# Optimization experiments

Hardware: AMD Instinct MI355X
Metric: run time of the kernel (lower is better)

Reference implementation:

```python
import jax, jax.numpy as jnp
import numpy as np

EPS = 1e-6
TEMPERATURE = 0.1
NEG_INF = -1.0e9

B, S, H = 8, 1024, 1024
M = 16384  # memory_size


def setup_inputs() -> dict:
    key = jax.random.key(0)
    ks = jax.random.split(key, 10)
    sc = 1.0 / np.sqrt(H)
    return {
        "hidden_states": jax.random.normal(ks[0], (B, S, H), jnp.float32),
        "Wk": jax.random.normal(ks[1], (H, H), jnp.float32) * sc,
        "bk": jax.random.normal(ks[2], (H,), jnp.float32) * 0.01,
        "Wv": jax.random.normal(ks[3], (H, H), jnp.float32) * sc,
        "bv": jax.random.normal(ks[4], (H,), jnp.float32) * 0.01,
        "Wo": jax.random.normal(ks[5], (H, H), jnp.float32) * sc,
        "bo": jax.random.normal(ks[6], (H,), jnp.float32) * 0.01,
        "memory_keys": jax.random.normal(ks[7], (M, H), jnp.float32),
        "memory_values": jax.random.normal(ks[8], (M, H), jnp.float32),
        "memory_usage": jax.random.randint(ks[9], (M,), 0, 3, jnp.int32),
    }


def _normalize(x):
    # matches torch: x * rsqrt(sum(x^2) + 1e-6)
    return x * jax.lax.rsqrt(jnp.sum(jnp.square(x), axis=-1, keepdims=True) + EPS)


def reference(hidden_states, Wk, bk, Wv, bv, Wo, bo,
              memory_keys, memory_values, memory_usage):
    # key projection + L2-ish normalization of queries
    q = hidden_states @ Wk.T + bk              # [B,S,H]
    qn = _normalize(q)
    mkn = _normalize(memory_keys)              # [M,H]
    # cosine-similarity attention over memory slots
    scores = jnp.einsum('bsh,mh->bsm', qn, mkn) / TEMPERATURE  # [B,S,M]
    mask = (memory_usage > 0).astype(scores.dtype)             # [M]
    scores = scores * mask + NEG_INF * (1.0 - mask)
    w = jax.nn.softmax(scores, axis=-1)                        # [B,S,M]
    retrieved = jnp.einsum('bsm,mh->bsh', w, memory_values)    # [B,S,H]
    return retrieved @ Wo.T + bo
```

## Files before the change

### kernel.cpp

```cpp
#include <hip/hip_runtime.h>
#include <hip/hip_bf16.h>
#include <stdint.h>
#include <stddef.h>

typedef __bf16 bf16_t;
typedef __attribute__((ext_vector_type(8))) __bf16 bf16x8;
typedef __attribute__((ext_vector_type(4))) __bf16 bf16x4;
typedef __attribute__((ext_vector_type(4))) float f32x4;

#define HDIM 1024
#define MSLOTS 16384
#define NROWS 8192

__device__ __forceinline__ void load16_lds(const void* g, void* l) {
  __builtin_amdgcn_global_load_lds((const __attribute__((address_space(1))) void*)g,
                                   (__attribute__((address_space(3))) void*)l, 16, 0, 0);
}

__global__ void init_compact(int* __restrict__ cmask) {
  int i = blockIdx.x * blockDim.x + threadIdx.x;
  if (i < MSLOTS) cmask[i] = 0;
}

__global__ void compact_scan(const int* __restrict__ usage, int* __restrict__ posmap,
                             int* __restrict__ cmask, int* __restrict__ smalls) {
  __shared__ int wtot[16], wbase[16];
  const int t = threadIdx.x;
  const int lane = t & 63, wid = t >> 6;
  const int base = t * 16;
  unsigned mask = 0;
  int c = 0;
  #pragma unroll
  for (int i = 0; i < 16; ++i) {
    if (usage[base + i] > 0) { mask |= (1u << i); ++c; }
  }
  int inc = c;
  #pragma unroll
  for (int d = 1; d < 64; d <<= 1) {
    int n = __shfl_up(inc, d);
    if (lane >= d) inc += n;
  }
  if (lane == 63) wtot[wid] = inc;
  __syncthreads();
  if (t == 0) {
    int acc = 0;
    #pragma unroll
    for (int w = 0; w < 16; ++w) { wbase[w] = acc; acc += wtot[w]; }
    smalls[0] = acc;
    smalls[1] = ((acc + 511) >> 9) << 9;
  }
  __syncthreads();
  int pos = wbase[wid] + inc - c;
  #pragma unroll
  for (int i = 0; i < 16; ++i) {
    if ((mask >> i) & 1u) {
      posmap[pos] = base + i;
      cmask[pos] = 1;
      ++pos;
    }
  }
}

__global__ void cvt_f32_bf16(const float* __restrict__ X, bf16_t* __restrict__ Y, int n8) {
  int i = blockIdx.x * blockDim.x + threadIdx.x;
  if (i >= n8) return;
  float4 a = ((const float4*)X)[2 * i];
  float4 b = ((const float4*)X)[2 * i + 1];
  bf16x8 o;
  o[0] = (bf16_t)a.x; o[1] = (bf16_t)a.y; o[2] = (bf16_t)a.z; o[3] = (bf16_t)a.w;
  o[4] = (bf16_t)b.x; o[5] = (bf16_t)b.y; o[6] = (bf16_t)b.z; o[7] = (bf16_t)b.w;
  ((bf16x8*)Y)[i] = o;
}

__global__ void normalize_rows(const float* __restrict__ X, bf16_t* __restrict__ Y) {
  __shared__ float part[4];
  const int t = threadIdx.x;
  const size_t row = blockIdx.x;
  float4 v = ((const float4*)(X + row * 1024))[t];
  float s = v.x * v.x + v.y * v.y + v.z * v.z + v.w * v.w;
  #pragma unroll
  for (int m = 32; m >= 1; m >>= 1) s += __shfl_xor(s, m);
  if ((t & 63) == 0) part[t >> 6] = s;
  __syncthreads();
  float tot = part[0] + part[1] + part[2] + part[3];
  float r = rsqrtf(tot + 1e-6f);
  bf16x4 o;
  o[0] = (bf16_t)(v.x * r); o[1] = (bf16_t)(v.y * r);
  o[2] = (bf16_t)(v.z * r); o[3] = (bf16_t)(v.w * r);
  *(bf16x4*)&Y[row * 1024 + t * 4] = o;
}

__global__ void normalize_gather(const float* __restrict__ mk, const int* __restrict__ posmap,
                                 const int* __restrict__ smalls, bf16_t* __restrict__ cmkn) {
  __shared__ float part[4];
  const int p = blockIdx.x;
  const int cnt = smalls[0], mpad = smalls[1];
  if (p >= mpad) return;
  const int t = threadIdx.x;
  if (p >= cnt) {
    bf16x4 z;
    z[0] = z[1] = z[2] = z[3] = (bf16_t)0.f;
    *(bf16x4*)&cmkn[(size_t)p * 1024 + t * 4] = z;
    return;
  }
  const int slot = posmap[p];
  float4 v = ((const float4*)(mk + (size_t)slot * 1024))[t];
  float s = v.x * v.x + v.y * v.y + v.z * v.z + v.w * v.w;
  #pragma unroll
  for (int m = 32; m >= 1; m >>= 1) s += __shfl_xor(s, m);
  if ((t & 63) == 0) part[t >> 6] = s;
  __syncthreads();
  float tot = part[0] + part[1] + part[2] + part[3];
  float r = rsqrtf(tot + 1e-6f);
  bf16x4 o;
  o[0] = (bf16_t)(v.x * r); o[1] = (bf16_t)(v.y * r);
  o[2] = (bf16_t)(v.z * r); o[3] = (bf16_t)(v.w * r);
  *(bf16x4*)&cmkn[(size_t)p * 1024 + t * 4] = o;
}

__global__ void transpose_gather(const float* __restrict__ mv, const int* __restrict__ posmap,
                                 const int* __restrict__ smalls, bf16_t* __restrict__ cVt) {
  __shared__ float tile[32][33];
  const int cnt = smalls[0], mpad = smalls[1];
  const int p0 = blockIdx.y * 32;
  if (p0 >= mpad) return;
  const int tx = threadIdx.x & 31, ty = threadIdx.x >> 5;
  const int h0 = blockIdx.x * 32;
  #pragma unroll
  for (int j = 0; j < 32; j += 8) {
    const int pos = p0 + ty + j;
    float val = 0.f;
    if (pos < cnt) val = mv[(size_t)posmap[pos] * 1024 + h0 + tx];
    tile[ty + j][tx] = val;
  }
  __syncthreads();
  #pragma unroll
  for (int j = 0; j < 32; j += 8)
    cVt[(size_t)(h0 + ty + j) * MSLOTS + p0 + tx] = (bf16_t)tile[tx][ty + j];
}

__global__ void zero_f32(float* __restrict__ p, int n4) {
  int i = blockIdx.x * blockDim.x + threadIdx.x;
  if (i < n4) ((float4*)p)[i] = (float4){0.f, 0.f, 0.f, 0.f};
}

__global__ void scale_cvt(const float* __restrict__ retrf, const float* __restrict__ den,
                          bf16_t* __restrict__ out, int n4) {
  int i = blockIdx.x * blockDim.x + threadIdx.x;
  if (i >= n4) return;
  float4 s = ((const float4*)retrf)[i];
  const int row = (i * 4) >> 10;
  const float r = 1.0f / den[row];
  bf16x4 o;
  o[0] = (bf16_t)(s.x * r); o[1] = (bf16_t)(s.y * r);
  o[2] = (bf16_t)(s.z * r); o[3] = (bf16_t)(s.w * r);
  ((bf16x4*)out)[i] = o;
}

__global__ void reduce_scale(const float* __restrict__ part, size_t partStride, int ks,
                             const float* __restrict__ den, bf16_t* __restrict__ out, int n4) {
  int i = blockIdx.x * blockDim.x + threadIdx.x;
  if (i >= n4) return;
  float4 s = ((const float4*)part)[i];
  for (int k = 1; k < ks; ++k) {
    float4 t = ((const float4*)(part + (size_t)k * partStride))[i];
    s.x += t.x; s.y += t.y; s.z += t.z; s.w += t.w;
  }
  const int row = (i * 4) >> 10;
  const float r = 1.0f / den[row];
  bf16x4 o;
  o[0] = (bf16_t)(s.x * r); o[1] = (bf16_t)(s.y * r);
  o[2] = (bf16_t)(s.z * r); o[3] = (bf16_t)(s.w * r);
  ((bf16x4*)out)[i] = o;
}

template <int EPI>
__global__ void gemm_bt(const bf16_t* __restrict__ A, const bf16_t* __restrict__ Bt,
                        int ldk, int kLenIn, int ldc,
                        const float* __restrict__ bias,
                        const int* __restrict__ cmask,
                        float* __restrict__ den,
                        float* __restrict__ outf, bf16_t* __restrict__ outb,
                        const int* __restrict__ smalls, int ks, size_t partStride) {
  __shared__ bf16_t lA[128 * 32];
  __shared__ bf16_t lB[128 * 32];
  const int t = threadIdx.x;
  const int lane = t & 63;
  const int wave = t >> 6;
  const int wm = (wave >> 1) << 6;
  const int wn = (wave & 1) << 6;
  const int lr = lane & 15;
  const int lq = lane >> 4;

  int bx = blockIdx.x, by = blockIdx.y, bz = blockIdx.z;
  {
    const unsigned nx = gridDim.x, ny = gridDim.y;
    if ((ny & 7u) == 0u) {
      unsigned lin = blockIdx.x + nx * (blockIdx.y + ny * blockIdx.z);
      unsigned ylow = lin & 7u;
      lin >>= 3;
      const unsigned nyh = ny >> 3;
      unsigned yhigh = lin % nyh;
      lin /= nyh;
      bx = lin % nx;
      bz = lin / nx;
      by = ylow + 8u * yhigh;
    }
  }

  int kLen = kLenIn;
  int kstart = 0;
  if (EPI == 1) {
    if (bx * 128 >= smalls[1]) return;
  }
  if (EPI == 3 || EPI == 4) {
    kLen = smalls[1] / ks;
    kstart = bz * kLen;
  }

  const int r0 = t >> 2;
  const int c0 = (t & 3) * 8;
  const bf16_t* pA0 = A + (size_t)(by * 128 + r0) * ldk + kstart + c0;
  const bf16_t* pA1 = pA0 + (size_t)64 * ldk;
  const bf16_t* pB0 = Bt + (size_t)(bx * 128 + r0) * ldk + kstart + c0;
  const bf16_t* pB1 = pB0 + (size_t)64 * ldk;

  f32x4 acc[4][4];
  #pragma unroll
  for (int i = 0; i < 4; ++i)
    #pragma unroll
    for (int j = 0; j < 4; ++j) acc[i][j] = (f32x4){0.f, 0.f, 0.f, 0.f};

  for (int k0 = 0; k0 < kLen; k0 += 32) {
    __syncthreads();
    load16_lds(pA0, &lA[t * 8]);
    load16_lds(pA1, &lA[2048 + t * 8]);
    load16_lds(pB0, &lB[t * 8]);
    load16_lds(pB1, &lB[2048 + t * 8]);
    pA0 += 32; pA1 += 32; pB0 += 32; pB1 += 32;
    __syncthreads();
    bf16x8 af[4], bfr[4];
    #pragma unroll
    for (int i = 0; i < 4; ++i)
      af[i] = *(const bf16x8*)&lA[(wm + i * 16 + lr) * 32 + lq * 8];
    #pragma unroll
    for (int j = 0; j < 4; ++j)
      bfr[j] = *(const bf16x8*)&lB[(wn + j * 16 + lr) * 32 + lq * 8];
    #pragma unroll
    for (int i = 0; i < 4; ++i)
      #pragma unroll
      for (int j = 0; j < 4; ++j)
        acc[i][j] = __builtin_amdgcn_mfma_f32_16x16x32_bf16(af[i], bfr[j], acc[i][j], 0, 0, 0);
  }

  const int colBase = bx * 128 + wn + lr;
  const int rowBase = by * 128 + wm + lq * 4;

  if (EPI == 4) outf += (size_t)bz * partStride;

  float rs[4][4];
  if (EPI == 1) {
    #pragma unroll
    for (int i = 0; i < 4; ++i)
      #pragma unroll
      for (int r = 0; r < 4; ++r) rs[i][r] = 0.f;
  }

  #pragma unroll
  for (int j = 0; j < 4; ++j) {
    const int col = colBase + j * 16;
    float bval = 0.f;
    bool ok = true;
    if (EPI == 0) bval = bias[col];
    if (EPI == 1) ok = cmask[col] > 0;
    #pragma unroll
    for (int i = 0; i < 4; ++i) {
      const int row = rowBase + i * 16;
      #pragma unroll
      for (int r = 0; r < 4; ++r) {
        const size_t idx = (size_t)(row + r) * ldc + col;
        float v = acc[i][j][r];
        if (EPI == 0) outf[idx] = v + bval;
        if (EPI == 1) {
          float e = ok ? exp2f(v * 14.426950408889634f) : 0.f;
          rs[i][r] += e;
          outb[idx] = (bf16_t)e;
        }
        if (EPI == 3) atomicAdd(&outf[idx], v);
        if (EPI == 4) outf[idx] = v;
      }
    }
  }

  if (EPI == 1) {
    #pragma unroll
    for (int i = 0; i < 4; ++i)
      #pragma unroll
      for (int r = 0; r < 4; ++r) {
        float s = rs[i][r];
        s += __shfl_xor(s, 1);
        s += __shfl_xor(s, 2);
        s += __shfl_xor(s, 4);
        s += __shfl_xor(s, 8);
        if (lr == 0) atomicAdd(&den[rowBase + i * 16 + r], s);
      }
  }
}

extern "C" void kernel_launch(void* const* d_in, const int* in_sizes, int n_in,
                              void* d_out, int out_size, void* d_ws, size_t ws_size,
                              hipStream_t stream) {
  const float* hs = (const float*)d_in[0];
  const float* Wk = (const float*)d_in[1];
  const float* bk = (const float*)d_in[2];
  const float* Wo = (const float*)d_in[5];
  const float* bo = (const float*)d_in[6];
  const float* mk = (const float*)d_in[7];
  const float* mv = (const float*)d_in[8];
  const int* usage = (const int*)d_in[9];
  float* out = (float*)d_out;

  char* ws = (char*)d_ws;
  size_t off = 0;
  auto alloc = [&](size_t b) -> void* {
    void* p = ws + off;
    off += (b + 255) & ~(size_t)255;
    return p;
  };
  bf16_t* cmkn = (bf16_t*)alloc((size_t)MSLOTS * HDIM * 2);
  bf16_t* cVt = (bf16_t*)alloc((size_t)HDIM * MSLOTS * 2);
  bf16_t* qnb = (bf16_t*)alloc((size_t)NROWS * HDIM * 2);
  bf16_t* retrb = (bf16_t*)alloc((size_t)NROWS * HDIM * 2);
  bf16_t* Wob = (bf16_t*)alloc((size_t)HDIM * HDIM * 2);
  float* den = (float*)alloc((size_t)NROWS * 4);
  int* posmap = (int*)alloc((size_t)MSLOTS * 4);
  int* cmask = (int*)alloc((size_t)MSLOTS * 4);
  int* smalls = (int*)alloc(256 * 4);
  const size_t fixed = off;

  int chunk = 128, ksplit = 4, partialMode = 0;
  {
    const int cc[8] = {4096, 4096, 2048, 2048, 1024, 1024, 512, 128};
    const int kk[8] = {4, 4, 8, 8, 8, 8, 16, 4};
    const int pp[8] = {1, 0, 1, 0, 1, 0, 0, 0};
    for (int ci = 0; ci < 8; ++ci) {
      size_t outBytes = pp[ci] ? (size_t)cc[ci] * HDIM * 4 * kk[ci] : (size_t)cc[ci] * HDIM * 4;
      size_t region = (size_t)cc[ci] * MSLOTS * 2 + outBytes;
      size_t phaseA = (size_t)NROWS * HDIM * 2 + (size_t)HDIM * HDIM * 2 +
                      (size_t)NROWS * HDIM * 4 + 1024;
      if (region < phaseA) region = phaseA;
      if (fixed + region <= ws_size) {
        chunk = cc[ci]; ksplit = kk[ci]; partialMode = pp[ci];
        break;
      }
    }
  }
  bf16_t* hsb = (bf16_t*)(ws + fixed);
  bf16_t* Wkb = (bf16_t*)(ws + fixed + (size_t)NROWS * HDIM * 2);
  float* qf = (float*)(ws + fixed + (size_t)NROWS * HDIM * 2 + (size_t)HDIM * HDIM * 2);
  bf16_t* P = (bf16_t*)(ws + fixed);
  float* retrf = (float*)(ws + fixed + (size_t)chunk * MSLOTS * 2);
  const size_t partStride = (size_t)chunk * HDIM;

  init_compact<<<MSLOTS / 256, 256, 0, stream>>>(cmask);
  compact_scan<<<1, 1024, 0, stream>>>(usage, posmap, cmask, smalls);
  cvt_f32_bf16<<<(NROWS * HDIM / 8 + 255) / 256, 256, 0, stream>>>(hs, hsb, NROWS * HDIM / 8);
  cvt_f32_bf16<<<(HDIM * HDIM / 8 + 255) / 256, 256, 0, stream>>>(Wk, Wkb, HDIM * HDIM / 8);
  cvt_f32_bf16<<<(HDIM * HDIM / 8 + 255) / 256, 256, 0, stream>>>(Wo, Wob, HDIM * HDIM / 8);
  normalize_gather<<<MSLOTS, 256, 0, stream>>>(mk, posmap, smalls, cmkn);
  transpose_gather<<<dim3(HDIM / 32, MSLOTS / 32), 256, 0, stream>>>(mv, posmap, smalls, cVt);

  gemm_bt<0><<<dim3(HDIM / 128, NROWS / 128), 256, 0, stream>>>(
      hsb, Wkb, HDIM, HDIM, HDIM, bk, nullptr, nullptr, qf, nullptr, smalls, 1, 0);
  normalize_rows<<<NROWS, 256, 0, stream>>>(qf, qnb);

  for (int c = 0; c < NROWS; c += chunk) {
    zero_f32<<<(chunk / 4 + 255) / 256, 256, 0, stream>>>(den, chunk / 4);
    gemm_bt<1><<<dim3(MSLOTS / 128, chunk / 128), 256, 0, stream>>>(
        qnb + (size_t)c * HDIM, cmkn, HDIM, HDIM, MSLOTS, nullptr, cmask, den, nullptr, P,
        smalls, 1, 0);
    if (partialMode) {
      gemm_bt<4><<<dim3(HDIM / 128, chunk / 128, ksplit), 256, 0, stream>>>(
          P, cVt, MSLOTS, 0, HDIM, nullptr, nullptr, nullptr, retrf, nullptr, smalls, ksplit,
          partStride);
      reduce_scale<<<(chunk * HDIM / 4 + 255) / 256, 256, 0, stream>>>(
          retrf, partStride, ksplit, den, retrb + (size_t)c * HDIM, chunk * HDIM / 4);
    } else {
      zero_f32<<<(chunk * HDIM / 4 + 255) / 256, 256, 0, stream>>>(retrf, chunk * HDIM / 4);
      gemm_bt<3><<<dim3(HDIM / 128, chunk / 128, ksplit), 256, 0, stream>>>(
          P, cVt, MSLOTS, 0, HDIM, nullptr, nullptr, nullptr, retrf, nullptr, smalls, ksplit,
          0);
      scale_cvt<<<(chunk * HDIM / 4 + 255) / 256, 256, 0, stream>>>(
          retrf, den, retrb + (size_t)c * HDIM, chunk * HDIM / 4);
    }
  }

  gemm_bt<0><<<dim3(HDIM / 128, NROWS / 128), 256, 0, stream>>>(
      retrb, Wob, HDIM, HDIM, HDIM, bo, nullptr, nullptr, out, nullptr, smalls, 1, 0);
}
```

Before: 828.6 us.

## Add 256x256-tile GEMM with 4-stage async LDS pipeline for attention GEMMs

Adds a new gemm256 kernel with 512 threads, 256x256 output tiles, and a 4-deep ring of LDS buffers filled by global_load_lds. Explicit vmcnt waits let loads for later K-steps overlap the MFMA work on the current step, and setprio is raised around the MFMA block. The two memory-attention GEMMs (scores+exp and P@V) now use this kernel, while the original gemm_bt is trimmed to the bias epilogue only. The minimum chunk grows to 256 rows. In exchange, LDS per block is large (128KB) and register pressure is high, which may limit occupancy, and the bigger tiles cut the number of blocks for the split-K P@V GEMM.

```diff
diff --git a/kernel.cpp b/kernel.cpp
--- a/kernel.cpp
+++ b/kernel.cpp
@@ -172,6 +172,152 @@
   o[0] = (bf16_t)(s.x * r); o[1] = (bf16_t)(s.y * r);
   o[2] = (bf16_t)(s.z * r); o[3] = (bf16_t)(s.w * r);
   ((bf16x4*)out)[i] = o;
+}
+
+template <int EPI>
+__global__ __launch_bounds__(512, 2)
+void gemm256(const bf16_t* __restrict__ A, const bf16_t* __restrict__ Bt,
+             int ldk, int kLenIn, int ldc,
+             const float* __restrict__ bias,
+             const int* __restrict__ cmask,
+             float* __restrict__ den,
+             float* __restrict__ outf, bf16_t* __restrict__ outb,
+             const int* __restrict__ smalls, int ks, size_t partStride) {
+  __shared__ bf16_t lA[4][256 * 32];
+  __shared__ bf16_t lB[4][256 * 32];
+  const int tid = threadIdx.x;
+  const int lane = tid & 63;
+  const int wave = tid >> 6;
+  const int wr = wave >> 2;
+  const int wc = wave & 3;
+  const int lr = lane & 15;
+  const int lq = lane >> 4;
+
+  int bx = blockIdx.x, by = blockIdx.y, bz = blockIdx.z;
+  {
+    const unsigned nx = gridDim.x, ny = gridDim.y;
+    if ((ny & 7u) == 0u) {
+      unsigned lin = blockIdx.x + nx * (blockIdx.y + ny * blockIdx.z);
+      unsigned ylow = lin & 7u;
+      lin >>= 3;
+      const unsigned nyh = ny >> 3;
+      unsigned yhigh = lin % nyh;
+      lin /= nyh;
+      bx = lin % nx;
+      bz = lin / nx;
+      by = ylow + 8u * yhigh;
+    }
+  }
+
+  int kLen = kLenIn;
+  int kstart = 0;
+  if (EPI == 1) {
+    if (bx * 256 >= smalls[1]) return;
+  }
+  if (EPI == 3 || EPI == 4) {
+    kLen = smalls[1] / ks;
+    kstart = bz * kLen;
+  }
+  const int nt = kLen >> 5;
+
+  const int srow = tid >> 2;
+  const int scol = (tid & 3) * 8;
+  const bf16_t* pA0 = A + (size_t)(by * 256 + srow) * ldk + kstart + scol;
+  const bf16_t* pA1 = pA0 + (size_t)128 * ldk;
+  const bf16_t* pB0 = Bt + (size_t)(bx * 256 + srow) * ldk + kstart + scol;
+  const bf16_t* pB1 = pB0 + (size_t)128 * ldk;
+
+  f32x4 acc[8][4];
+  #pragma unroll
+  for (int m = 0; m < 8; ++m)
+    #pragma unroll
+    for (int n = 0; n < 4; ++n) acc[m][n] = (f32x4){0.f, 0.f, 0.f, 0.f};
+
+#define STAGE(tt)                                              \
+  do {                                                         \
+    const int _b = (tt) & 3;                                   \
+    const size_t _ko = (size_t)(tt) * 32;                      \
+    load16_lds(pA0 + _ko, &lA[_b][tid * 8]);                   \
+    load16_lds(pA1 + _ko, &lA[_b][4096 + tid * 8]);            \
+    load16_lds(pB0 + _ko, &lB[_b][tid * 8]);                   \
+    load16_lds(pB1 + _ko, &lB[_b][4096 + tid * 8]);            \
+  } while (0)
+
+  if (nt > 0) STAGE(0);
+  if (nt > 1) STAGE(1);
+  if (nt > 2) STAGE(2);
+
+  for (int t = 0; t < nt; ++t) {
+    if (t + 3 < nt) STAGE(t + 3);
+    const int rem = nt - 1 - t;
+    if (rem >= 3)      asm volatile("s_waitcnt vmcnt(12)" ::: "memory");
+    else if (rem == 2) asm volatile("s_waitcnt vmcnt(8)" ::: "memory");
+    else if (rem == 1) asm volatile("s_waitcnt vmcnt(4)" ::: "memory");
+    else               asm volatile("s_waitcnt vmcnt(0)" ::: "memory");
+    __builtin_amdgcn_s_barrier();
+    __builtin_amdgcn_sched_barrier(0);
+    const int b = t & 3;
+    const bf16_t* bAp = &lA[b][0];
+    const bf16_t* bBp = &lB[b][0];
+    bf16x8 bfr[4];
+    #pragma unroll
+    for (int n = 0; n < 4; ++n)
+      bfr[n] = *(const bf16x8*)&bBp[(wc * 64 + n * 16 + lr) * 32 + lq * 8];
+    __builtin_amdgcn_s_setprio(1);
+    #pragma unroll
+    for (int m = 0; m < 8; ++m) {
+      bf16x8 af = *(const bf16x8*)&bAp[(wr * 128 + m * 16 + lr) * 32 + lq * 8];
+      #pragma unroll
+      for (int n = 0; n < 4; ++n)
+        acc[m][n] = __builtin_amdgcn_mfma_f32_16x16x32_bf16(af, bfr[n], acc[m][n], 0, 0, 0);
+    }
+    __builtin_amdgcn_s_setprio(0);
+    __builtin_amdgcn_sched_barrier(0);
+    __builtin_amdgcn_s_barrier();
+    __builtin_amdgcn_sched_barrier(0);
+  }
+#undef STAGE
+
+  const int colBase = bx * 256 + wc * 64 + lr;
+  const int rowBase = by * 256 + wr * 128 + lq * 4;
+
+  if (EPI == 1) {
+    bool ok[4];
+    #pragma unroll
+    for (int n = 0; n < 4; ++n) ok[n] = cmask[colBase + n * 16] > 0;
+    #pragma unroll
+    for (int m = 0; m < 8; ++m) {
+      #pragma unroll
+      for (int r = 0; r < 4; ++r) {
+        const int row = rowBase + m * 16 + r;
+        float s = 0.f;
+        #pragma unroll
+        for (int n = 0; n < 4; ++n) {
+          float e = ok[n] ? exp2f(acc[m][n][r] * 14.426950408889634f) : 0.f;
+          s += e;
+          outb[(size_t)row * ldc + colBase + n * 16] = (bf16_t)e;
+        }
+        s += __shfl_xor(s, 1);
+        s += __shfl_xor(s, 2);
+        s += __shfl_xor(s, 4);
+        s += __shfl_xor(s, 8);
+        if (lr == 0) atomicAdd(&den[row], s);
+      }
+    }
+  }
+  if (EPI == 3 || EPI == 4) {
+    if (EPI == 4) outf += (size_t)bz * partStride;
+    #pragma unroll
+    for (int m = 0; m < 8; ++m)
+      #pragma unroll
+      for (int n = 0; n < 4; ++n)
+        #pragma unroll
+        for (int r = 0; r < 4; ++r) {
+          const size_t idx = (size_t)(rowBase + m * 16 + r) * ldc + colBase + n * 16;
+          if (EPI == 3) atomicAdd(&outf[idx], acc[m][n][r]);
+          else outf[idx] = acc[m][n][r];
+        }
+  }
 }
 
 template <int EPI>
@@ -210,13 +356,6 @@
 
   int kLen = kLenIn;
   int kstart = 0;
-  if (EPI == 1) {
-    if (bx * 128 >= smalls[1]) return;
-  }
-  if (EPI == 3 || EPI == 4) {
-    kLen = smalls[1] / ks;
-    kstart = bz * kLen;
-  }
 
   const int r0 = t >> 2;
   const int c0 = (t & 3) * 8;
@@ -256,23 +395,11 @@
   const int colBase = bx * 128 + wn + lr;
   const int rowBase = by * 128 + wm + lq * 4;
 
-  if (EPI == 4) outf += (size_t)bz * partStride;
-
-  float rs[4][4];
-  if (EPI == 1) {
-    #pragma unroll
-    for (int i = 0; i < 4; ++i)
-      #pragma unroll
-      for (int r = 0; r < 4; ++r) rs[i][r] = 0.f;
-  }
-
   #pragma unroll
   for (int j = 0; j < 4; ++j) {
     const int col = colBase + j * 16;
     float bval = 0.f;
-    bool ok = true;
     if (EPI == 0) bval = bias[col];
-    if (EPI == 1) ok = cmask[col] > 0;
     #pragma unroll
     for (int i = 0; i < 4; ++i) {
       const int row = rowBase + i * 16;
@@ -281,29 +408,8 @@
         const size_t idx = (size_t)(row + r) * ldc + col;
         float v = acc[i][j][r];
         if (EPI == 0) outf[idx] = v + bval;
-        if (EPI == 1) {
-          float e = ok ? exp2f(v * 14.426950408889634f) : 0.f;
-          rs[i][r] += e;
-          outb[idx] = (bf16_t)e;
-        }
-        if (EPI == 3) atomicAdd(&outf[idx], v);
-        if (EPI == 4) outf[idx] = v;
       }
     }
-  }
-
-  if (EPI == 1) {
-    #pragma unroll
-    for (int i = 0; i < 4; ++i)
-      #pragma unroll
-      for (int r = 0; r < 4; ++r) {
-        float s = rs[i][r];
-        s += __shfl_xor(s, 1);
-        s += __shfl_xor(s, 2);
-        s += __shfl_xor(s, 4);
-        s += __shfl_xor(s, 8);
-        if (lr == 0) atomicAdd(&den[rowBase + i * 16 + r], s);
-      }
   }
 }
 
@@ -338,9 +444,9 @@
   int* smalls = (int*)alloc(256 * 4);
   const size_t fixed = off;
 
-  int chunk = 128, ksplit = 4, partialMode = 0;
+  int chunk = 256, ksplit = 4, partialMode = 0;
   {
-    const int cc[8] = {4096, 4096, 2048, 2048, 1024, 1024, 512, 128};
+    const int cc[8] = {4096, 4096, 2048, 2048, 1024, 1024, 512, 256};
     const int kk[8] = {4, 4, 8, 8, 8, 8, 16, 4};
     const int pp[8] = {1, 0, 1, 0, 1, 0, 0, 0};
     for (int ci = 0; ci < 8; ++ci) {
@@ -376,18 +482,18 @@
 
   for (int c = 0; c < NROWS; c += chunk) {
     zero_f32<<<(chunk / 4 + 255) / 256, 256, 0, stream>>>(den, chunk / 4);
-    gemm_bt<1><<<dim3(MSLOTS / 128, chunk / 128), 256, 0, stream>>>(
+    gemm256<1><<<dim3(MSLOTS / 256, chunk / 256), 512, 0, stream>>>(
         qnb + (size_t)c * HDIM, cmkn, HDIM, HDIM, MSLOTS, nullptr, cmask, den, nullptr, P,
         smalls, 1, 0);
     if (partialMode) {
-      gemm_bt<4><<<dim3(HDIM / 128, chunk / 128, ksplit), 256, 0, stream>>>(
+      gemm256<4><<<dim3(HDIM / 256, chunk / 256, ksplit), 512, 0, stream>>>(
           P, cVt, MSLOTS, 0, HDIM, nullptr, nullptr, nullptr, retrf, nullptr, smalls, ksplit,
           partStride);
       reduce_scale<<<(chunk * HDIM / 4 + 255) / 256, 256, 0, stream>>>(
           retrf, partStride, ksplit, den, retrb + (size_t)c * HDIM, chunk * HDIM / 4);
     } else {
       zero_f32<<<(chunk * HDIM / 4 + 255) / 256, 256, 0, stream>>>(retrf, chunk * HDIM / 4);
-      gemm_bt<3><<<dim3(HDIM / 128, chunk / 128, ksplit), 256, 0, stream>>>(
+      gemm256<3><<<dim3(HDIM / 256, chunk / 256, ksplit), 512, 0, stream>>>(
           P, cVt, MSLOTS, 0, HDIM, nullptr, nullptr, nullptr, retrf, nullptr, smalls, ksplit,
           0);
       scale_cvt<<<(chunk * HDIM / 4 + 255) / 256, 256, 0, stream>>>(
```

Result: slower. 918.7 us (+10.9%).
